# Optimization experiments

Measured on AMD Instinct MI355X. Metric: run time of the kernel, lower is better.

Reference implementation:

```python
import jax, jax.numpy as jnp
import numpy as np

B, D, H = 16384, 1024, 1024


def setup_inputs() -> dict:
    key = jax.random.key(0)
    ks = jax.random.split(key, 6)
    s = 1.0 / np.sqrt(D)
    return {
        "x": jax.random.normal(ks[0], (B, D), jnp.float32),
        "h_prev": jax.random.normal(ks[1], (B, H), jnp.float32),
        "c_prev": jax.random.normal(ks[2], (B, H), jnp.float32),
        "dynamic_weight": jax.random.uniform(ks[3], (B, H), jnp.float32),
        # stacked gate weights: order [i, f, o, c, s] along first axis
        "Wx": jax.random.normal(ks[4], (5 * H, D), jnp.float32) * s,
        "bx": jnp.zeros((5 * H,), jnp.float32),
        "Uh": jax.random.normal(ks[5], (5 * H, H), jnp.float32) * s,
        "bh": jnp.zeros((5 * H,), jnp.float32),
    }


def reference(x, h_prev, c_prev, dynamic_weight, Wx, bx, Uh, bh):
    # two fused GEMMs covering all 10 original nn.Linear calls
    gates = (jnp.einsum('bd,gd->bg', x, Wx) + bx
             + jnp.einsum('bh,gh->bg', h_prev, Uh) + bh)  # [B, 5H]
    gi, gf, go, gc, gs = jnp.split(gates, 5, axis=-1)
    i_t = jax.nn.sigmoid(gi)
    f_t = jax.nn.sigmoid(gf)
    o_t = jax.nn.sigmoid(go)
    c_hat = jnp.tanh(gc)
    s_t = jax.nn.sigmoid(gs) * dynamic_weight
    c_t = f_t * c_prev + i_t * c_hat * s_t
    h_t = o_t * jnp.tanh(c_t)
    return h_t, c_t
```

## Files before the change

kernel.cpp:

```cpp
#include <hip/hip_runtime.h>
#include <hip/hip_bf16.h>

#define B_ROWS 16384
#define KDIM   2048
#define NDIM   5120
#define HDIM   1024

#define BM 256
#define BN 320
#define BK 32
#define NKT (KDIM / BK)
#define A_BYTES (BM * BK * 2)
#define W_BYTES (BN * BK * 2)
#define BUFSZ   (A_BYTES + W_BYTES)
#define NBUF  4
#define LDS_BYTES (NBUF * BUFSZ)

typedef __attribute__((ext_vector_type(8))) short short8;
typedef __attribute__((ext_vector_type(4))) float f32x4;

__device__ __forceinline__ void async_cp16(const void* g, void* l) {
  __builtin_amdgcn_global_load_lds(
      (const __attribute__((address_space(1))) void*)g,
      (__attribute__((address_space(3))) void*)l,
      16, 0, 0);
}

__global__ void detect_dtype(const unsigned short* __restrict__ p, int* flag) {
  __shared__ int cnt;
  if (threadIdx.x == 0) cnt = 0;
  __syncthreads();
  int h = 0;
  for (int i = threadIdx.x; i < 2048; i += 256) {
    int e = (p[i] >> 7) & 0xFF;
    if (e >= 137) h++;
  }
  atomicAdd(&cnt, h);
  __syncthreads();
  if (threadIdx.x == 0) *flag = (cnt >= 4) ? 1 : 0;
}

__global__ void pack_pair_f32(const float* __restrict__ s0, const float* __restrict__ s1,
                              __hip_bfloat16* __restrict__ dst, const int* __restrict__ flag,
                              long rbase, long total) {
  if (*flag == 0) return;
  long idx = ((long)blockIdx.x * blockDim.x + threadIdx.x) * 8;
  if (idx >= total) return;
  int  k = (int)(idx & (KDIM - 1));
  long r = (idx >> 11) + rbase;
  const float* s = (k < 1024) ? (s0 + r * 1024 + k) : (s1 + r * 1024 + (k - 1024));
  float4 v0 = ((const float4*)s)[0];
  float4 v1 = ((const float4*)s)[1];
  union { short8 v; __hip_bfloat16 e[8]; } u;
  u.e[0] = __float2bfloat16(v0.x); u.e[1] = __float2bfloat16(v0.y);
  u.e[2] = __float2bfloat16(v0.z); u.e[3] = __float2bfloat16(v0.w);
  u.e[4] = __float2bfloat16(v1.x); u.e[5] = __float2bfloat16(v1.y);
  u.e[6] = __float2bfloat16(v1.z); u.e[7] = __float2bfloat16(v1.w);
  *(short8*)(dst + idx) = u.v;
}

__global__ __launch_bounds__(512, 2) void gemm_fused(
    const __hip_bfloat16* __restrict__ Abf, const __hip_bfloat16* __restrict__ Wbf,
    const void* __restrict__ xr, const void* __restrict__ hr,
    const void* __restrict__ Wxr, const void* __restrict__ Uhr,
    const void* __restrict__ cpr, const void* __restrict__ dwr,
    const void* __restrict__ bxr, const void* __restrict__ bhr,
    float* __restrict__ out, const int* __restrict__ flag, int row_base) {
  extern __shared__ char lds[];

  const int tid = threadIdx.x;
  const int w   = tid >> 6;
  const int l   = tid & 63;

  const int nb  = gridDim.x;
  const int q8  = nb >> 3;
  const int sw  = (blockIdx.x & 7) * q8 + (blockIdx.x >> 3);
  const int m0l = (sw >> 4) * BM;
  const int h0  = (sw & 15) * 64;

  const int wm = w >> 2;
  const int wn = w & 3;

  const int fl = *flag;
  const int dc = (l & 3) ^ ((l >> 3) & 3);

  const __hip_bfloat16 *srcA0, *srcA1;
  long dA;
  {
    const int r0 = m0l + w * 32 + (l >> 2);
    if (fl) {
      srcA0 = Abf + (long)r0 * KDIM + dc * 8;
      srcA1 = Abf + (long)(r0 + 16) * KDIM + dc * 8;
      dA = 1024;
    } else {
      srcA0 = (const __hip_bfloat16*)xr + (long)(row_base + r0) * 1024 + dc * 8;
      srcA1 = (const __hip_bfloat16*)xr + (long)(row_base + r0 + 16) * 1024 + dc * 8;
      dA = (const __hip_bfloat16*)hr - (const __hip_bfloat16*)xr;
    }
  }

  const bool has3 = (w < 4);
  const int  jw0  = has3 ? (3 * w)     : (2 * w + 4);
  const int  jw1  = has3 ? (3 * w + 1) : (2 * w + 5);
  const int  jw2  = has3 ? (3 * w + 2) : (2 * w + 5);
  const __hip_bfloat16 *srcW0, *srcW1, *srcW2;
  long dW;
  {
    const __hip_bfloat16* wbase;
    long strW;
    if (fl) { wbase = Wbf; strW = KDIM; dW = 1024; }
    else {
      wbase = (const __hip_bfloat16*)Wxr; strW = 1024;
      dW = (const __hip_bfloat16*)Uhr - (const __hip_bfloat16*)Wxr;
    }
    const int j0g = jw0 % 5, j0w = jw0 / 5;
    const int j1g = jw1 % 5, j1w = jw1 / 5;
    const int j2g = jw2 % 5, j2w = jw2 / 5;
    srcW0 = wbase + ((long)j0g * 1024 + h0 + j0w * 16 + (l >> 2)) * strW + dc * 8;
    srcW1 = wbase + ((long)j1g * 1024 + h0 + j1w * 16 + (l >> 2)) * strW + dc * 8;
    srcW2 = wbase + ((long)j2g * 1024 + h0 + j2w * 16 + (l >> 2)) * strW + dc * 8;
  }

#define STAGE(T) do {                                                        \
    const int  b_  = (T) & 3;                                                \
    const int  k0_ = (T) * BK;                                               \
    const long koA_ = (k0_ < 1024) ? (long)k0_ : (dA + (k0_ - 1024));        \
    const long koW_ = (k0_ < 1024) ? (long)k0_ : (dW + (k0_ - 1024));        \
    char* lb_ = lds + b_ * BUFSZ;                                            \
    async_cp16(srcA0 + koA_, lb_ + w * 2048 + l * 16);                       \
    async_cp16(srcA1 + koA_, lb_ + w * 2048 + 1024 + l * 16);                \
    async_cp16(srcW0 + koW_, lb_ + A_BYTES + jw0 * 1024 + l * 16);           \
    async_cp16(srcW1 + koW_, lb_ + A_BYTES + jw1 * 1024 + l * 16);           \
    if (has3)                                                                \
      async_cp16(srcW2 + koW_, lb_ + A_BYTES + jw2 * 1024 + l * 16);         \
  } while (0)

  f32x4 acc[8][5] = {};
  const int frow  = l & 15;
  const int swz   = ((l >> 4) ^ ((frow >> 1) & 3)) << 4;
  const int aoff0 = (wm * 128 + frow) * 64;
  const int woff0 = A_BYTES + (wn * 80 + frow) * 64;

#define COMPUTE(T) do {                                                      \
    const char* ba_ = lds + ((T) & 3) * BUFSZ;                               \
    short8 af_[8], wf_[5];                                                   \
    _Pragma("unroll")                                                        \
    for (int nj = 0; nj < 5; ++nj)                                           \
      wf_[nj] = *(const short8*)(ba_ + woff0 + nj * 1024 + swz);             \
    _Pragma("unroll")                                                        \
    for (int mi = 0; mi < 8; ++mi)                                           \
      af_[mi] = *(const short8*)(ba_ + aoff0 + mi * 1024 + swz);             \
    __builtin_amdgcn_s_setprio(1);                                           \
    _Pragma("unroll")                                                        \
    for (int mi = 0; mi < 8; ++mi)                                           \
      _Pragma("unroll")                                                      \
      for (int nj = 0; nj < 5; ++nj)                                         \
        acc[mi][nj] = __builtin_amdgcn_mfma_f32_16x16x32_bf16(               \
            af_[mi], wf_[nj], acc[mi][nj], 0, 0, 0);                         \
    __builtin_amdgcn_s_setprio(0);                                           \
  } while (0)

  STAGE(0); STAGE(1); STAGE(2);

  for (int t = 0; t < NKT - 3; ++t) {
    __builtin_amdgcn_s_barrier();
    __builtin_amdgcn_sched_barrier(0);
    STAGE(t + 3);
    if (has3) { asm volatile("s_waitcnt vmcnt(15)" ::: "memory"); }
    else      { asm volatile("s_waitcnt vmcnt(12)" ::: "memory"); }
    __builtin_amdgcn_sched_barrier(0);
    __builtin_amdgcn_s_barrier();
    __builtin_amdgcn_sched_barrier(0);
    COMPUTE(t);
  }
  for (int t = NKT - 3; t < NKT; ++t) {
    __builtin_amdgcn_s_barrier();
    asm volatile("s_waitcnt vmcnt(0)" ::: "memory");
    __builtin_amdgcn_sched_barrier(0);
    __builtin_amdgcn_s_barrier();
    __builtin_amdgcn_sched_barrier(0);
    COMPUTE(t);
  }

#undef STAGE
#undef COMPUTE

  const int hh = h0 + wn * 16 + frow;
  float bsum[5];
#pragma unroll
  for (int g = 0; g < 5; ++g) {
    if (fl) {
      bsum[g] = ((const float*)bxr)[g * 1024 + hh] + ((const float*)bhr)[g * 1024 + hh];
    } else {
      bsum[g] = __bfloat162float(((const __hip_bfloat16*)bxr)[g * 1024 + hh])
              + __bfloat162float(((const __hip_bfloat16*)bhr)[g * 1024 + hh]);
    }
  }
  const long orow0 = (long)row_base + m0l + wm * 128 + (l >> 4) * 4;
  float* outc = out + (long)B_ROWS * HDIM;
#pragma unroll
  for (int mi = 0; mi < 8; ++mi) {
#pragma unroll
    for (int r = 0; r < 4; ++r) {
      const long idx = (orow0 + mi * 16 + r) * HDIM + hh;
      float cp, dv;
      if (fl) {
        cp = ((const float*)cpr)[idx];
        dv = ((const float*)dwr)[idx];
      } else {
        cp = __bfloat162float(((const __hip_bfloat16*)cpr)[idx]);
        dv = __bfloat162float(((const __hip_bfloat16*)dwr)[idx]);
      }
      const float gi = acc[mi][0][r] + bsum[0];
      const float gf = acc[mi][1][r] + bsum[1];
      const float go = acc[mi][2][r] + bsum[2];
      const float gc = acc[mi][3][r] + bsum[3];
      const float gs = acc[mi][4][r] + bsum[4];
      const float it = 1.f / (1.f + __expf(-gi));
      const float ft = 1.f / (1.f + __expf(-gf));
      const float ot = 1.f / (1.f + __expf(-go));
      const float ch = tanhf(gc);
      const float st = (1.f / (1.f + __expf(-gs))) * dv;
      const float ct = ft * cp + it * ch * st;
      out[idx]  = ot * tanhf(ct);
      outc[idx] = ct;
    }
  }
}

extern "C" void kernel_launch(void* const* d_in, const int* in_sizes, int n_in,
                              void* d_out, int out_size, void* d_ws, size_t ws_size,
                              hipStream_t stream) {
  const void* x      = d_in[0];
  const void* h_prev = d_in[1];
  const void* c_prev = d_in[2];
  const void* dw     = d_in[3];
  const void* Wx     = d_in[4];
  const void* bx     = d_in[5];
  const void* Uh     = d_in[6];
  const void* bh     = d_in[7];

  static int lds_attr_done = 0;
  if (!lds_attr_done) {
    hipFuncSetAttribute((const void*)gemm_fused,
                        hipFuncAttributeMaxDynamicSharedMemorySize, LDS_BYTES);
    lds_attr_done = 1;
  }

  const size_t wbf_bytes = (size_t)NDIM * KDIM * 2;
  int nc = 32;
  for (int c = 1; c <= 32; c <<= 1) {
    size_t need = 256 + wbf_bytes
                + (size_t)(B_ROWS / c) * KDIM * 2;
    if (need <= ws_size) { nc = c; break; }
  }
  const long rows = B_ROWS / nc;

  char* ws = (char*)d_ws;
  int* flag = (int*)ws;
  __hip_bfloat16* Wbf = (__hip_bfloat16*)(ws + 256);
  __hip_bfloat16* Abf = (__hip_bfloat16*)(ws + 256 + wbf_bytes);

  detect_dtype<<<1, 256, 0, stream>>>((const unsigned short*)x, flag);

  pack_pair_f32<<<(int)(((long)NDIM * KDIM) / 2048), 256, 0, stream>>>(
      (const float*)Wx, (const float*)Uh, Wbf, flag, 0, (long)NDIM * KDIM);

  for (int c = 0; c < nc; ++c) {
    long rbase = c * rows;
    pack_pair_f32<<<(int)rows, 256, 0, stream>>>(
        (const float*)x, (const float*)h_prev, Abf, flag, rbase, rows * KDIM);
    const int nblocks = (int)(16 * (rows / BM));
    gemm_fused<<<nblocks, 512, LDS_BYTES, stream>>>(
        Abf, Wbf, x, h_prev, Wx, Uh, c_prev, dw, bx, bh,
        (float*)d_out, flag, (int)rbase);
  }
}
```

Baseline: 706.9 us.

## Pack weights in gate-interleaved tile order and switch GEMM to a 2D grid

Result: no change. 710.7 us (+0.5%).

```diff
diff --git a/kernel.cpp b/kernel.cpp
--- a/kernel.cpp
+++ b/kernel.cpp
@@ -59,6 +59,30 @@
   *(short8*)(dst + idx) = u.v;
 }
 
+__global__ void pack_w_gate(const float* __restrict__ Wx, const float* __restrict__ Uh,
+                            __hip_bfloat16* __restrict__ dst, const int* __restrict__ flag) {
+  if (*flag == 0) return;
+  long idx = ((long)blockIdx.x * blockDim.x + threadIdx.x) * 8;
+  const int k  = (int)(idx & (KDIM - 1));
+  const int np = (int)(idx >> 11);
+  const int hg = np / 320;
+  const int r3 = np - hg * 320;
+  const int wg = r3 / 80;
+  const int r8 = r3 - wg * 80;
+  const int g  = r8 >> 4;
+  const int t  = r8 & 15;
+  const long row = (long)g * 1024 + hg * 64 + wg * 16 + t;
+  const float* s = (k < 1024) ? (Wx + row * 1024 + k) : (Uh + row * 1024 + (k - 1024));
+  float4 v0 = ((const float4*)s)[0];
+  float4 v1 = ((const float4*)s)[1];
+  union { short8 v; __hip_bfloat16 e[8]; } u;
+  u.e[0] = __float2bfloat16(v0.x); u.e[1] = __float2bfloat16(v0.y);
+  u.e[2] = __float2bfloat16(v0.z); u.e[3] = __float2bfloat16(v0.w);
+  u.e[4] = __float2bfloat16(v1.x); u.e[5] = __float2bfloat16(v1.y);
+  u.e[6] = __float2bfloat16(v1.z); u.e[7] = __float2bfloat16(v1.w);
+  *(short8*)(dst + idx) = u.v;
+}
+
 __global__ __launch_bounds__(512, 2) void gemm_fused(
     const __hip_bfloat16* __restrict__ Abf, const __hip_bfloat16* __restrict__ Wbf,
     const void* __restrict__ xr, const void* __restrict__ hr,
@@ -72,11 +96,9 @@
   const int w   = tid >> 6;
   const int l   = tid & 63;
 
-  const int nb  = gridDim.x;
-  const int q8  = nb >> 3;
-  const int sw  = (blockIdx.x & 7) * q8 + (blockIdx.x >> 3);
-  const int m0l = (sw >> 4) * BM;
-  const int h0  = (sw & 15) * 64;
+  const int hg  = blockIdx.x;
+  const int m0l = blockIdx.y * BM;
+  const int h0  = hg * 64;
 
   const int wm = w >> 2;
   const int wn = w & 3;
@@ -100,25 +122,25 @@
   }
 
   const bool has3 = (w < 4);
-  const int  jw0  = has3 ? (3 * w)     : (2 * w + 4);
-  const int  jw1  = has3 ? (3 * w + 1) : (2 * w + 5);
-  const int  jw2  = has3 ? (3 * w + 2) : (2 * w + 5);
+  const int  jw0  = w;
+  const int  jw1  = w + 8;
+  const int  jw2  = has3 ? (w + 16) : (w + 8);
   const __hip_bfloat16 *srcW0, *srcW1, *srcW2;
   long dW;
-  {
-    const __hip_bfloat16* wbase;
-    long strW;
-    if (fl) { wbase = Wbf; strW = KDIM; dW = 1024; }
-    else {
-      wbase = (const __hip_bfloat16*)Wxr; strW = 1024;
-      dW = (const __hip_bfloat16*)Uhr - (const __hip_bfloat16*)Wxr;
-    }
+  if (fl) {
+    srcW0 = Wbf + ((long)hg * 320 + jw0 * 16 + (l >> 2)) * KDIM + dc * 8;
+    srcW1 = Wbf + ((long)hg * 320 + jw1 * 16 + (l >> 2)) * KDIM + dc * 8;
+    srcW2 = Wbf + ((long)hg * 320 + jw2 * 16 + (l >> 2)) * KDIM + dc * 8;
+    dW = 1024;
+  } else {
+    const __hip_bfloat16* wbase = (const __hip_bfloat16*)Wxr;
+    dW = (const __hip_bfloat16*)Uhr - (const __hip_bfloat16*)Wxr;
     const int j0g = jw0 % 5, j0w = jw0 / 5;
     const int j1g = jw1 % 5, j1w = jw1 / 5;
     const int j2g = jw2 % 5, j2w = jw2 / 5;
-    srcW0 = wbase + ((long)j0g * 1024 + h0 + j0w * 16 + (l >> 2)) * strW + dc * 8;
-    srcW1 = wbase + ((long)j1g * 1024 + h0 + j1w * 16 + (l >> 2)) * strW + dc * 8;
-    srcW2 = wbase + ((long)j2g * 1024 + h0 + j2w * 16 + (l >> 2)) * strW + dc * 8;
+    srcW0 = wbase + ((long)j0g * 1024 + h0 + j0w * 16 + (l >> 2)) * 1024 + dc * 8;
+    srcW1 = wbase + ((long)j1g * 1024 + h0 + j1w * 16 + (l >> 2)) * 1024 + dc * 8;
+    srcW2 = wbase + ((long)j2g * 1024 + h0 + j2w * 16 + (l >> 2)) * 1024 + dc * 8;
   }
 
 #define STAGE(T) do {                                                        \
@@ -263,15 +285,15 @@
 
   detect_dtype<<<1, 256, 0, stream>>>((const unsigned short*)x, flag);
 
-  pack_pair_f32<<<(int)(((long)NDIM * KDIM) / 2048), 256, 0, stream>>>(
-      (const float*)Wx, (const float*)Uh, Wbf, flag, 0, (long)NDIM * KDIM);
+  pack_w_gate<<<(int)(((long)NDIM * KDIM) / 2048), 256, 0, stream>>>(
+      (const float*)Wx, (const float*)Uh, Wbf, flag);
 
   for (int c = 0; c < nc; ++c) {
     long rbase = c * rows;
     pack_pair_f32<<<(int)rows, 256, 0, stream>>>(
         (const float*)x, (const float*)h_prev, Abf, flag, rbase, rows * KDIM);
-    const int nblocks = (int)(16 * (rows / BM));
-    gemm_fused<<<nblocks, 512, LDS_BYTES, stream>>>(
+    dim3 grid(NDIM / BN, (int)(rows / BM));
+    gemm_fused<<<grid, 512, LDS_BYTES, stream>>>(
         Abf, Wbf, x, h_prev, Wx, Uh, c_prev, dw, bx, bh,
         (float*)d_out, flag, (int)rbase);
   }
```
